# Performance work log

Measured on AMD Instinct MI355X. Metric: run time of the kernel, lower is better.

Reference implementation:

```python
import jax, jax.numpy as jnp
import numpy as np

D_MODEL = 1024


def setup_inputs() -> dict:
    key = jax.random.key(0)
    kx, kq, kk, kv = jax.random.split(key, 4)
    x = jax.random.normal(kx, (4, 2048, D_MODEL), dtype=jnp.float32)
    s = 1.0 / np.sqrt(D_MODEL)
    # torch nn.Linear weight is [out, in]; y = x @ W.T
    Wq = jax.random.normal(kq, (D_MODEL, D_MODEL), dtype=jnp.float32) * s
    Wk = jax.random.normal(kk, (D_MODEL, D_MODEL), dtype=jnp.float32) * s
    Wv = jax.random.normal(kv, (D_MODEL, D_MODEL), dtype=jnp.float32) * s
    return {"x": x, "Wq": Wq, "Wk": Wk, "Wv": Wv}


def reference(x, Wq, Wk, Wv):
    # Linear projections (no bias): [b, s, d]
    Q = jnp.einsum("bsd,ed->bse", x, Wq)
    K = jnp.einsum("bsd,ed->bse", x, Wk)
    V = jnp.einsum("bsd,ed->bse", x, Wv)
    d_k = Q.shape[-1]
    scores = jnp.einsum("bqd,bkd->bqk", Q, K) / jnp.sqrt(jnp.asarray(d_k, Q.dtype))
    weights = jax.nn.softmax(scores, axis=-1)
    return jnp.einsum("bqk,bkd->bqd", weights, V)
```

## Files before the change

kernel.cpp:

```cpp
#include <hip/hip_runtime.h>
#include <hip/hip_bf16.h>

using bf16 = __hip_bfloat16;
typedef __attribute__((ext_vector_type(8))) short short8;
typedef __attribute__((ext_vector_type(16))) float f32x16;

__global__ __launch_bounds__(256) void cast_all(const float* __restrict__ x,
                                                const float* __restrict__ Wq,
                                                const float* __restrict__ Wk,
                                                const float* __restrict__ Wv,
                                                bf16* __restrict__ xb, bf16* __restrict__ Wb) {
  const int b = blockIdx.x;
  const float* src;
  bf16* dst;
  if (b < 8192) {
    src = x + (size_t)b * 1024;
    dst = xb + (size_t)b * 1024;
  } else if (b < 9216) {
    src = Wq + (size_t)(b - 8192) * 1024;
    dst = Wb + (size_t)(b - 8192) * 1024;
  } else if (b < 10240) {
    src = Wk + (size_t)(b - 9216) * 1024;
    dst = Wb + (size_t)(b - 8192) * 1024;
  } else {
    src = Wv + (size_t)(b - 10240) * 1024;
    dst = Wb + (size_t)(b - 8192) * 1024;
  }
  const int i = threadIdx.x * 4;
  const float4 f = *(const float4*)(src + i);
  bf16 h[4];
  h[0] = __float2bfloat16(f.x);
  h[1] = __float2bfloat16(f.y);
  h[2] = __float2bfloat16(f.z);
  h[3] = __float2bfloat16(f.w);
  *(uint2*)(dst + i) = *(const uint2*)h;
}

template <class Epi>
__device__ __forceinline__ void gemm_nt(const bf16* __restrict__ A, const bf16* __restrict__ B,
                                        int lda, int ldb, int K, int m0, int n0, Epi epi) {
  constexpr int SLOT = 24576;
  __shared__ char smem[3 * SLOT];
  const int t = threadIdx.x;
  const int lane = t & 63;
  const int wave = t >> 6;
  const int wm = (wave >> 2) * 64;
  const int wn = (wave & 3) * 64;
  const int rl = lane & 31;
  const int grp = lane >> 5;

  f32x16 acc[2][2];
#pragma unroll
  for (int i = 0; i < 2; ++i)
#pragma unroll
    for (int j = 0; j < 2; ++j)
#pragma unroll
      for (int r = 0; r < 16; ++r) acc[i][j][r] = 0.f;

  const bf16* gA0;
  {
    const int row = t >> 2;
    const int f = (row + (row >> 2)) & 3;
    gA0 = A + (size_t)(m0 + row) * lda + ((((t & 3) ^ f)) << 3);
  }
  const bf16* gB[2];
#pragma unroll
  for (int j = 0; j < 2; ++j) {
    const int s = j * 512 + t;
    const int row = s >> 2;
    const int f = (row + (row >> 2)) & 3;
    gB[j] = B + (size_t)(n0 + row) * ldb + ((((s & 3) ^ f)) << 3);
  }

  auto stage = [&](int kt, int slot) {
    char* base = smem + slot * SLOT;
    bf16* As = (bf16*)base;
    bf16* Bs = (bf16*)(base + 8192);
    const int k0 = kt * 32;
    __builtin_amdgcn_global_load_lds(
        (const __attribute__((address_space(1))) unsigned int*)(gA0 + k0),
        (__attribute__((address_space(3))) unsigned int*)(As + wave * 512), 16, 0, 0);
#pragma unroll
    for (int j = 0; j < 2; ++j)
      __builtin_amdgcn_global_load_lds(
          (const __attribute__((address_space(1))) unsigned int*)(gB[j] + k0),
          (__attribute__((address_space(3))) unsigned int*)(Bs + (j * 512 + wave * 64) * 8), 16, 0, 0);
  };

  const int NT = K >> 5;

  stage(0, 0);
  stage(1, 1);
  asm volatile("s_waitcnt vmcnt(3)" ::: "memory");
  __builtin_amdgcn_s_barrier();
  __builtin_amdgcn_sched_barrier(0);

  int sr = 0;
  int ss = 2;
  for (int kt = 0; kt < NT; ++kt) {
    const char* base = smem + sr * SLOT;
    const bf16* As = (const bf16*)base;
    const bf16* Bs = (const bf16*)(base + 8192);

    if (kt + 2 < NT) stage(kt + 2, ss);

    short8 af[2][2], bv[2][2];
#pragma unroll
    for (int ks = 0; ks < 2; ++ks) {
      const int kb = ks * 2 + grp;
#pragma unroll
      for (int mt = 0; mt < 2; ++mt) {
        const int rowa = wm + mt * 32 + rl;
        const int fa = (rowa + (rowa >> 2)) & 3;
        af[ks][mt] = *(const short8*)(As + rowa * 32 + ((kb ^ fa) << 3));
        const int rowb = wn + mt * 32 + rl;
        const int fb = (rowb + (rowb >> 2)) & 3;
        bv[ks][mt] = *(const short8*)(Bs + rowb * 32 + ((kb ^ fb) << 3));
      }
    }
    __builtin_amdgcn_sched_barrier(0);
    asm volatile("s_waitcnt lgkmcnt(0)" ::: "memory");
    __builtin_amdgcn_sched_barrier(0);
    __builtin_amdgcn_s_setprio(1);
#pragma unroll
    for (int ks = 0; ks < 2; ++ks)
#pragma unroll
      for (int mt = 0; mt < 2; ++mt)
#pragma unroll
        for (int nt = 0; nt < 2; ++nt)
          acc[mt][nt] = __builtin_amdgcn_mfma_f32_32x32x16_bf16(af[ks][mt], bv[ks][nt],
                                                                acc[mt][nt], 0, 0, 0);
    __builtin_amdgcn_s_setprio(0);
    __builtin_amdgcn_sched_barrier(0);
    if (kt + 1 < NT) {
      if (kt + 2 < NT) {
        asm volatile("s_waitcnt vmcnt(3)" ::: "memory");
      } else {
        asm volatile("s_waitcnt vmcnt(0)" ::: "memory");
      }
      __builtin_amdgcn_s_barrier();
      __builtin_amdgcn_sched_barrier(0);
    }
    sr = (sr == 2) ? 0 : sr + 1;
    ss = (ss == 2) ? 0 : ss + 1;
  }
  __syncthreads();

  epi(acc, m0, n0, wm, wn, lane, wave, smem);
}

__device__ __forceinline__ int c_row(int reg, int lane) {
  return (reg & 3) + 8 * (reg >> 2) + 4 * (lane >> 5);
}

template <class F>
__device__ __forceinline__ void for_each_c(const f32x16 (&acc)[2][2], int wm, int wn, int lane,
                                           F f) {
  const int rl = lane & 31;
#pragma unroll
  for (int mt = 0; mt < 2; ++mt)
#pragma unroll
    for (int nt = 0; nt < 2; ++nt)
#pragma unroll
      for (int reg = 0; reg < 16; ++reg)
        f(wm + mt * 32 + c_row(reg, lane), wn + nt * 32 + rl, acc[mt][nt][reg]);
}

__global__ __launch_bounds__(512, 4) void proj_kernel(const bf16* __restrict__ xb,
                                                      const bf16* __restrict__ Wb,
                                                      bf16* __restrict__ Qb,
                                                      bf16* __restrict__ Kb,
                                                      bf16* __restrict__ Vt) {
  const int id = blockIdx.y * 12 + blockIdx.x;
  const int g = id & 7, s = id >> 3;
  const int m0 = (g * 8 + (s & 7)) * 128;
  const int n0 = (s >> 3) * 256;
  gemm_nt(xb, Wb, 1024, 1024, 1024, m0, n0,
          [=](const f32x16 (&acc)[2][2], int m0, int n0, int wm, int wn, int lane, int wave,
              char* smem) {
    if (n0 < 2048) {
      bf16* dst = (n0 < 1024) ? Qb : Kb;
      const int nb = (n0 < 1024) ? n0 : (n0 - 1024);
      for_each_c(acc, wm, wn, lane, [&](int m, int n, float v) {
        dst[(size_t)(m0 + m) * 1024 + nb + n] = __float2bfloat16(v);
      });
    } else {
      bf16* T = (bf16*)(smem) + wave * 2304;
      const int rl = lane & 31;
      const int g4 = 4 * (lane >> 5);
      const int mbase = m0 + wm;
      const int bb = mbase >> 11;
      const int sbase = mbase & 2047;
      const int nvbase = n0 - 2048 + wn;
#pragma unroll
      for (int p = 0; p < 2; ++p) {
#pragma unroll
        for (int mt = 0; mt < 2; ++mt)
#pragma unroll
          for (int q = 0; q < 4; ++q) {
            bf16 h4[4];
#pragma unroll
            for (int r = 0; r < 4; ++r) h4[r] = __float2bfloat16(acc[mt][p][4 * q + r]);
            *(uint2*)(T + rl * 72 + mt * 32 + 8 * q + g4) = *(const uint2*)h4;
          }
        asm volatile("s_waitcnt lgkmcnt(0)" ::: "memory");
#pragma unroll
        for (int i = 0; i < 4; ++i) {
          const int nl = i * 8 + (lane >> 3);
          const int ml = (lane & 7) * 8;
          const short8 val = *(const short8*)(T + nl * 72 + ml);
          *(short8*)(Vt + ((size_t)bb * 1024 + nvbase + p * 32 + nl) * 2048 + sbase + ml) = val;
        }
        asm volatile("s_waitcnt lgkmcnt(0)" ::: "memory");
      }
    }
  });
}

__global__ __launch_bounds__(512, 4) void qk_exp_kernel(const bf16* __restrict__ Qb,
                                                        const bf16* __restrict__ Kb,
                                                        bf16* __restrict__ E,
                                                        float* __restrict__ Lpart) {
  const int z = blockIdx.y;
  const int id2 = blockIdx.x;
  const int g = id2 & 7, s = id2 >> 3;
  const int m0 = ((g & 3) * 4 + (s & 3)) * 128;
  const int n0 = ((g >> 2) * 4 + (s >> 2)) * 256;
  const bf16* A = Qb + (size_t)z * 2048 * 1024;
  const bf16* B = Kb + (size_t)z * 2048 * 1024;
  bf16* Ez = E + (size_t)z * 2048 * 2048;
  float* Lz = Lpart + (size_t)z * 8 * 2048;
  gemm_nt(A, B, 1024, 1024, 1024, m0, n0,
          [=](const f32x16 (&acc)[2][2], int m0, int n0, int wm, int wn, int lane, int wave,
              char* smem) {
    float* Lp = (float*)smem;
    const int rl = lane & 31;
#pragma unroll
    for (int mt = 0; mt < 2; ++mt)
#pragma unroll
      for (int reg = 0; reg < 16; ++reg) {
        const int mr = wm + mt * 32 + c_row(reg, lane);
        float s2 = 0.f;
#pragma unroll
        for (int nt = 0; nt < 2; ++nt) {
          const float e = __expf(acc[mt][nt][reg] * 0.03125f);
          Ez[(size_t)(m0 + mr) * 2048 + n0 + wn + nt * 32 + rl] = __float2bfloat16(e);
          s2 += e;
        }
        s2 += __shfl_xor(s2, 1, 64);
        s2 += __shfl_xor(s2, 2, 64);
        s2 += __shfl_xor(s2, 4, 64);
        s2 += __shfl_xor(s2, 8, 64);
        s2 += __shfl_xor(s2, 16, 64);
        if (rl == 0) Lp[mr * 4 + (wave & 3)] = s2;
      }
    __syncthreads();
    const int t = threadIdx.x;
    if (t < 128)
      Lz[(n0 >> 8) * 2048 + m0 + t] =
          Lp[t * 4 + 0] + Lp[t * 4 + 1] + Lp[t * 4 + 2] + Lp[t * 4 + 3];
  });
}

__global__ __launch_bounds__(512, 4) void pv_kernel(const bf16* __restrict__ E,
                                                    const bf16* __restrict__ Vt,
                                                    const float* __restrict__ Lpart,
                                                    float* __restrict__ out) {
  const int z = blockIdx.y;
  const int id2 = blockIdx.x;
  const int g = id2 & 7, s = id2 >> 3;
  const int m0 = ((g & 3) * 4 + (s & 3)) * 128;
  const int n0 = ((g >> 2) * 2 + (s >> 2)) * 256;
  const bf16* A = E + (size_t)z * 2048 * 2048;
  const bf16* B = Vt + (size_t)z * 1024 * 2048;
  const float* Lz = Lpart + (size_t)z * 8 * 2048;
  float* oz = out + (size_t)z * 2048 * 1024;
  gemm_nt(A, B, 2048, 2048, 2048, m0, n0,
          [=](const f32x16 (&acc)[2][2], int m0, int n0, int wm, int wn, int lane, int wave,
              char* smem) {
    float* Lsm = (float*)smem;
    const int t = threadIdx.x;
    if (t < 128) {
      float s2 = 0.f;
#pragma unroll
      for (int i = 0; i < 8; ++i) s2 += Lz[(size_t)i * 2048 + m0 + t];
      Lsm[t] = 1.f / s2;
    }
    __syncthreads();
    const int rl = lane & 31;
#pragma unroll
    for (int mt = 0; mt < 2; ++mt)
#pragma unroll
      for (int reg = 0; reg < 16; ++reg) {
        const int ml = wm + mt * 32 + c_row(reg, lane);
        const float il = Lsm[ml];
#pragma unroll
        for (int nt = 0; nt < 2; ++nt)
          oz[(size_t)(m0 + ml) * 1024 + n0 + wn + nt * 32 + rl] = acc[mt][nt][reg] * il;
      }
  });
}

extern "C" void kernel_launch(void* const* d_in, const int* in_sizes, int n_in,
                              void* d_out, int out_size, void* d_ws, size_t ws_size,
                              hipStream_t stream) {
  const float* x = (const float*)d_in[0];
  const float* Wq = (const float*)d_in[1];
  const float* Wk = (const float*)d_in[2];
  const float* Wv = (const float*)d_in[3];
  float* out = (float*)d_out;

  char* w = (char*)d_ws;
  bf16* xb = (bf16*)w; w += (size_t)8192 * 1024 * 2;
  bf16* Wb = (bf16*)w; w += (size_t)3072 * 1024 * 2;
  bf16* Qb = (bf16*)w; w += (size_t)8192 * 1024 * 2;
  bf16* Kb = (bf16*)w; w += (size_t)8192 * 1024 * 2;
  bf16* Vt = (bf16*)w; w += (size_t)8192 * 1024 * 2;
  bf16* E  = (bf16*)w; w += (size_t)4 * 2048 * 2048 * 2;
  float* Lpart = (float*)w; w += (size_t)4 * 8 * 2048 * 4;

  cast_all<<<11264, 256, 0, stream>>>(x, Wq, Wk, Wv, xb, Wb);

  proj_kernel<<<dim3(12, 64), 512, 0, stream>>>(xb, Wb, Qb, Kb, Vt);

  qk_exp_kernel<<<dim3(128, 4), 512, 0, stream>>>(Qb, Kb, E, Lpart);

  pv_kernel<<<dim3(64, 4), 512, 0, stream>>>(E, Vt, Lpart, out);
}
```

Baseline: 229.5 us.

## Software-pipeline LDS fragment reads with MFMA using double-buffered register fragments

Restructures the projection GEMM main loop, unrolling it by two and keeping two register fragment sets. Each iteration loads the next tile's A/B fragments from LDS while MFMAs run on the current set. The goal is to hide LDS read latency behind matrix math instead of stalling on lgkmcnt(0) before every MFMA batch. It costs extra VGPRs for the second fragment set and assumes an even number of K tiles.

```diff
diff --git a/kernel.cpp b/kernel.cpp
--- a/kernel.cpp
+++ b/kernel.cpp
@@ -87,6 +87,41 @@
           (__attribute__((address_space(3))) unsigned int*)(Bs + (j * 512 + wave * 64) * 8), 16, 0, 0);
   };
 
+  struct Frags {
+    short8 af[2][2];
+    short8 bv[2][2];
+  };
+  auto read_frags = [&](int slot, Frags& f) {
+    const char* base = smem + slot * SLOT;
+    const bf16* As = (const bf16*)base;
+    const bf16* Bs = (const bf16*)(base + 8192);
+#pragma unroll
+    for (int ks = 0; ks < 2; ++ks) {
+      const int kb = ks * 2 + grp;
+#pragma unroll
+      for (int mt = 0; mt < 2; ++mt) {
+        const int rowa = wm + mt * 32 + rl;
+        const int fa = (rowa + (rowa >> 2)) & 3;
+        f.af[ks][mt] = *(const short8*)(As + rowa * 32 + ((kb ^ fa) << 3));
+        const int rowb = wn + mt * 32 + rl;
+        const int fb = (rowb + (rowb >> 2)) & 3;
+        f.bv[ks][mt] = *(const short8*)(Bs + rowb * 32 + ((kb ^ fb) << 3));
+      }
+    }
+  };
+  auto mfma_all = [&](const Frags& f) {
+    __builtin_amdgcn_s_setprio(1);
+#pragma unroll
+    for (int ks = 0; ks < 2; ++ks)
+#pragma unroll
+      for (int mt = 0; mt < 2; ++mt)
+#pragma unroll
+        for (int nt = 0; nt < 2; ++nt)
+          acc[mt][nt] = __builtin_amdgcn_mfma_f32_32x32x16_bf16(f.af[ks][mt], f.bv[ks][nt],
+                                                                acc[mt][nt], 0, 0, 0);
+    __builtin_amdgcn_s_setprio(0);
+  };
+
   const int NT = K >> 5;
 
   stage(0, 0);
@@ -94,55 +129,34 @@
   asm volatile("s_waitcnt vmcnt(3)" ::: "memory");
   __builtin_amdgcn_s_barrier();
   __builtin_amdgcn_sched_barrier(0);
-
-  int sr = 0;
-  int ss = 2;
-  for (int kt = 0; kt < NT; ++kt) {
-    const char* base = smem + sr * SLOT;
-    const bf16* As = (const bf16*)base;
-    const bf16* Bs = (const bf16*)(base + 8192);
-
-    if (kt + 2 < NT) stage(kt + 2, ss);
-
-    short8 af[2][2], bv[2][2];
-#pragma unroll
-    for (int ks = 0; ks < 2; ++ks) {
-      const int kb = ks * 2 + grp;
-#pragma unroll
-      for (int mt = 0; mt < 2; ++mt) {
-        const int rowa = wm + mt * 32 + rl;
-        const int fa = (rowa + (rowa >> 2)) & 3;
-        af[ks][mt] = *(const short8*)(As + rowa * 32 + ((kb ^ fa) << 3));
-        const int rowb = wn + mt * 32 + rl;
-        const int fb = (rowb + (rowb >> 2)) & 3;
-        bv[ks][mt] = *(const short8*)(Bs + rowb * 32 + ((kb ^ fb) << 3));
-      }
-    }
+  Frags fA, fB;
+  read_frags(0, fA);
+
+  int s0 = 0;
+  for (int kt = 0; kt < NT; kt += 2) {
+    const int s1 = (s0 == 2) ? 0 : s0 + 1;
+    const int s2 = (s1 == 2) ? 0 : s1 + 1;
+    if (kt + 2 < NT) {
+      stage(kt + 2, s2);
+      asm volatile("s_waitcnt vmcnt(3) lgkmcnt(0)" ::: "memory");
+    } else {
+      asm volatile("s_waitcnt vmcnt(0) lgkmcnt(0)" ::: "memory");
+    }
+    __builtin_amdgcn_s_barrier();
     __builtin_amdgcn_sched_barrier(0);
-    asm volatile("s_waitcnt lgkmcnt(0)" ::: "memory");
+    read_frags(s1, fB);
+    mfma_all(fA);
+    if (kt + 3 < NT) {
+      stage(kt + 3, s0);
+      asm volatile("s_waitcnt vmcnt(3) lgkmcnt(0)" ::: "memory");
+    } else {
+      asm volatile("s_waitcnt vmcnt(0) lgkmcnt(0)" ::: "memory");
+    }
+    __builtin_amdgcn_s_barrier();
     __builtin_amdgcn_sched_barrier(0);
-    __builtin_amdgcn_s_setprio(1);
-#pragma unroll
-    for (int ks = 0; ks < 2; ++ks)
-#pragma unroll
-      for (int mt = 0; mt < 2; ++mt)
-#pragma unroll
-        for (int nt = 0; nt < 2; ++nt)
-          acc[mt][nt] = __builtin_amdgcn_mfma_f32_32x32x16_bf16(af[ks][mt], bv[ks][nt],
-                                                                acc[mt][nt], 0, 0, 0);
-    __builtin_amdgcn_s_setprio(0);
-    __builtin_amdgcn_sched_barrier(0);
-    if (kt + 1 < NT) {
-      if (kt + 2 < NT) {
-        asm volatile("s_waitcnt vmcnt(3)" ::: "memory");
-      } else {
-        asm volatile("s_waitcnt vmcnt(0)" ::: "memory");
-      }
-      __builtin_amdgcn_s_barrier();
-      __builtin_amdgcn_sched_barrier(0);
-    }
-    sr = (sr == 2) ? 0 : sr + 1;
-    ss = (ss == 2) ? 0 : ss + 1;
+    if (kt + 2 < NT) read_frags(s2, fA);
+    mfma_all(fB);
+    s0 = s2;
   }
   __syncthreads();
 
```

Result: slower. 629.4 us (+174.3%).

## Use 128x128 tiles for PV GEMM and batch rows in cast kernel

Applied to the files above, without the earlier changes.

Templates the shared GEMM on the N tile width so the PV kernel can run 128x128 tiles with 256 threads, doubling its block count to better fill the GPU's compute units. The load distribution, LDS slot size and wait counts are adjusted for the smaller tile. The cast kernel now converts four rows per block to cut block launch overhead. Smaller tiles reduce per-block data reuse and add more global traffic for the PV operands.

```diff
diff --git a/kernel.cpp b/kernel.cpp
--- a/kernel.cpp
+++ b/kernel.cpp
@@ -10,42 +10,49 @@
                                                 const float* __restrict__ Wk,
                                                 const float* __restrict__ Wv,
                                                 bf16* __restrict__ xb, bf16* __restrict__ Wb) {
-  const int b = blockIdx.x;
+  const int r0 = blockIdx.x << 2;
   const float* src;
   bf16* dst;
-  if (b < 8192) {
-    src = x + (size_t)b * 1024;
-    dst = xb + (size_t)b * 1024;
-  } else if (b < 9216) {
-    src = Wq + (size_t)(b - 8192) * 1024;
-    dst = Wb + (size_t)(b - 8192) * 1024;
-  } else if (b < 10240) {
-    src = Wk + (size_t)(b - 9216) * 1024;
-    dst = Wb + (size_t)(b - 8192) * 1024;
+  if (r0 < 8192) {
+    src = x + (size_t)r0 * 1024;
+    dst = xb + (size_t)r0 * 1024;
+  } else if (r0 < 9216) {
+    src = Wq + (size_t)(r0 - 8192) * 1024;
+    dst = Wb + (size_t)(r0 - 8192) * 1024;
+  } else if (r0 < 10240) {
+    src = Wk + (size_t)(r0 - 9216) * 1024;
+    dst = Wb + (size_t)(r0 - 8192) * 1024;
   } else {
-    src = Wv + (size_t)(b - 10240) * 1024;
-    dst = Wb + (size_t)(b - 8192) * 1024;
-  }
-  const int i = threadIdx.x * 4;
-  const float4 f = *(const float4*)(src + i);
-  bf16 h[4];
-  h[0] = __float2bfloat16(f.x);
-  h[1] = __float2bfloat16(f.y);
-  h[2] = __float2bfloat16(f.z);
-  h[3] = __float2bfloat16(f.w);
-  *(uint2*)(dst + i) = *(const uint2*)h;
-}
-
-template <class Epi>
+    src = Wv + (size_t)(r0 - 10240) * 1024;
+    dst = Wb + (size_t)(r0 - 8192) * 1024;
+  }
+  const int i = threadIdx.x * 16;
+#pragma unroll
+  for (int q = 0; q < 4; ++q) {
+    const float4 f = *(const float4*)(src + i + q * 4);
+    bf16 h[4];
+    h[0] = __float2bfloat16(f.x);
+    h[1] = __float2bfloat16(f.y);
+    h[2] = __float2bfloat16(f.z);
+    h[3] = __float2bfloat16(f.w);
+    *(uint2*)(dst + i + q * 4) = *(const uint2*)h;
+  }
+}
+
+template <int BN, class Epi>
 __device__ __forceinline__ void gemm_nt(const bf16* __restrict__ A, const bf16* __restrict__ B,
                                         int lda, int ldb, int K, int m0, int n0, Epi epi) {
-  constexpr int SLOT = 24576;
+  constexpr int THREADS = BN * 2;
+  constexpr int NA = 8192 / (THREADS * 16);
+  constexpr int NB = (BN * 64) / (THREADS * 16);
+  constexpr int L = NA + NB;
+  constexpr int SLOT = (128 + BN) * 64;
   __shared__ char smem[3 * SLOT];
   const int t = threadIdx.x;
   const int lane = t & 63;
   const int wave = t >> 6;
-  const int wm = (wave >> 2) * 64;
-  const int wn = (wave & 3) * 64;
+  const int wm = (BN == 256) ? (wave >> 2) * 64 : (wave >> 1) * 64;
+  const int wn = (BN == 256) ? (wave & 3) * 64 : (wave & 1) * 64;
   const int rl = lane & 31;
   const int grp = lane >> 5;
 
@@ -57,16 +64,18 @@
 #pragma unroll
       for (int r = 0; r < 16; ++r) acc[i][j][r] = 0.f;
 
-  const bf16* gA0;
-  {
-    const int row = t >> 2;
+  const bf16* gA[NA];
+#pragma unroll
+  for (int j = 0; j < NA; ++j) {
+    const int s = j * THREADS + t;
+    const int row = s >> 2;
     const int f = (row + (row >> 2)) & 3;
-    gA0 = A + (size_t)(m0 + row) * lda + ((((t & 3) ^ f)) << 3);
-  }
-  const bf16* gB[2];
-#pragma unroll
-  for (int j = 0; j < 2; ++j) {
-    const int s = j * 512 + t;
+    gA[j] = A + (size_t)(m0 + row) * lda + ((((s & 3) ^ f)) << 3);
+  }
+  const bf16* gB[NB];
+#pragma unroll
+  for (int j = 0; j < NB; ++j) {
+    const int s = j * THREADS + t;
     const int row = s >> 2;
     const int f = (row + (row >> 2)) & 3;
     gB[j] = B + (size_t)(n0 + row) * ldb + ((((s & 3) ^ f)) << 3);
@@ -77,32 +86,41 @@
     bf16* As = (bf16*)base;
     bf16* Bs = (bf16*)(base + 8192);
     const int k0 = kt * 32;
-    __builtin_amdgcn_global_load_lds(
-        (const __attribute__((address_space(1))) unsigned int*)(gA0 + k0),
-        (__attribute__((address_space(3))) unsigned int*)(As + wave * 512), 16, 0, 0);
-#pragma unroll
-    for (int j = 0; j < 2; ++j)
+#pragma unroll
+    for (int j = 0; j < NA; ++j)
+      __builtin_amdgcn_global_load_lds(
+          (const __attribute__((address_space(1))) unsigned int*)(gA[j] + k0),
+          (__attribute__((address_space(3))) unsigned int*)(As + (j * THREADS + wave * 64) * 8),
+          16, 0, 0);
+#pragma unroll
+    for (int j = 0; j < NB; ++j)
       __builtin_amdgcn_global_load_lds(
           (const __attribute__((address_space(1))) unsigned int*)(gB[j] + k0),
-          (__attribute__((address_space(3))) unsigned int*)(Bs + (j * 512 + wave * 64) * 8), 16, 0, 0);
+          (__attribute__((address_space(3))) unsigned int*)(Bs + (j * THREADS + wave * 64) * 8),
+          16, 0, 0);
   };
 
   const int NT = K >> 5;
 
   stage(0, 0);
   stage(1, 1);
-  asm volatile("s_waitcnt vmcnt(3)" ::: "memory");
+  if constexpr (BN == 256) {
+    asm volatile("s_waitcnt vmcnt(3)" ::: "memory");
+  } else {
+    asm volatile("s_waitcnt vmcnt(4)" ::: "memory");
+  }
   __builtin_amdgcn_s_barrier();
   __builtin_amdgcn_sched_barrier(0);
 
-  int sr = 0;
-  int ss = 2;
+  int s0 = 0;
   for (int kt = 0; kt < NT; ++kt) {
-    const char* base = smem + sr * SLOT;
+    const int s1 = (s0 == 2) ? 0 : s0 + 1;
+    const int s2 = (s1 == 2) ? 0 : s1 + 1;
+    const char* base = smem + s0 * SLOT;
     const bf16* As = (const bf16*)base;
     const bf16* Bs = (const bf16*)(base + 8192);
 
-    if (kt + 2 < NT) stage(kt + 2, ss);
+    if (kt + 2 < NT) stage(kt + 2, s2);
 
     short8 af[2][2], bv[2][2];
 #pragma unroll
@@ -134,15 +152,18 @@
     __builtin_amdgcn_sched_barrier(0);
     if (kt + 1 < NT) {
       if (kt + 2 < NT) {
-        asm volatile("s_waitcnt vmcnt(3)" ::: "memory");
+        if constexpr (BN == 256) {
+          asm volatile("s_waitcnt vmcnt(3)" ::: "memory");
+        } else {
+          asm volatile("s_waitcnt vmcnt(4)" ::: "memory");
+        }
       } else {
         asm volatile("s_waitcnt vmcnt(0)" ::: "memory");
       }
       __builtin_amdgcn_s_barrier();
       __builtin_amdgcn_sched_barrier(0);
     }
-    sr = (sr == 2) ? 0 : sr + 1;
-    ss = (ss == 2) ? 0 : ss + 1;
+    s0 = s1;
   }
   __syncthreads();
 
@@ -175,7 +196,7 @@
   const int g = id & 7, s = id >> 3;
   const int m0 = (g * 8 + (s & 7)) * 128;
   const int n0 = (s >> 3) * 256;
-  gemm_nt(xb, Wb, 1024, 1024, 1024, m0, n0,
+  gemm_nt<256>(xb, Wb, 1024, 1024, 1024, m0, n0,
           [=](const f32x16 (&acc)[2][2], int m0, int n0, int wm, int wn, int lane, int wave,
               char* smem) {
     if (n0 < 2048) {
@@ -230,7 +251,7 @@
   const bf16* B = Kb + (size_t)z * 2048 * 1024;
   bf16* Ez = E + (size_t)z * 2048 * 2048;
   float* Lz = Lpart + (size_t)z * 8 * 2048;
-  gemm_nt(A, B, 1024, 1024, 1024, m0, n0,
+  gemm_nt<256>(A, B, 1024, 1024, 1024, m0, n0,
           [=](const f32x16 (&acc)[2][2], int m0, int n0, int wm, int wn, int lane, int wave,
               char* smem) {
     float* Lp = (float*)smem;
@@ -262,7 +283,7 @@
   });
 }
 
-__global__ __launch_bounds__(512, 4) void pv_kernel(const bf16* __restrict__ E,
+__global__ __launch_bounds__(256, 4) void pv_kernel(const bf16* __restrict__ E,
                                                     const bf16* __restrict__ Vt,
                                                     const float* __restrict__ Lpart,
                                                     float* __restrict__ out) {
@@ -270,12 +291,12 @@
   const int id2 = blockIdx.x;
   const int g = id2 & 7, s = id2 >> 3;
   const int m0 = ((g & 3) * 4 + (s & 3)) * 128;
-  const int n0 = ((g >> 2) * 2 + (s >> 2)) * 256;
+  const int n0 = ((g >> 2) * 4 + (s >> 2)) * 128;
   const bf16* A = E + (size_t)z * 2048 * 2048;
   const bf16* B = Vt + (size_t)z * 1024 * 2048;
   const float* Lz = Lpart + (size_t)z * 8 * 2048;
   float* oz = out + (size_t)z * 2048 * 1024;
-  gemm_nt(A, B, 2048, 2048, 2048, m0, n0,
+  gemm_nt<128>(A, B, 2048, 2048, 2048, m0, n0,
           [=](const f32x16 (&acc)[2][2], int m0, int n0, int wm, int wn, int lane, int wave,
               char* smem) {
     float* Lsm = (float*)smem;
@@ -319,11 +340,11 @@
   bf16* E  = (bf16*)w; w += (size_t)4 * 2048 * 2048 * 2;
   float* Lpart = (float*)w; w += (size_t)4 * 8 * 2048 * 4;
 
-  cast_all<<<11264, 256, 0, stream>>>(x, Wq, Wk, Wv, xb, Wb);
+  cast_all<<<2816, 256, 0, stream>>>(x, Wq, Wk, Wv, xb, Wb);
 
   proj_kernel<<<dim3(12, 64), 512, 0, stream>>>(xb, Wb, Qb, Kb, Vt);
 
   qk_exp_kernel<<<dim3(128, 4), 512, 0, stream>>>(Qb, Kb, E, Lpart);
 
-  pv_kernel<<<dim3(64, 4), 512, 0, stream>>>(E, Vt, Lpart, out);
-}
+  pv_kernel<<<dim3(128, 4), 256, 0, stream>>>(E, Vt, Lpart, out);
+}
```

Measured after the change: 235.7 us. 2.7% more time.
